# Kernel optimization log

Hardware: AMD Instinct MI355X
Metric: run time of the kernel (lower is better)

The kernel has to match this reference:

```python
import jax, jax.numpy as jnp
import numpy as np

N, I, H = 32, 64, 128
B, T = 16, 256


def setup_inputs() -> dict:
    key = jax.random.key(0)
    k1, k2, k3, k4, k5 = jax.random.split(key, 5)
    stdv = 1.0 / np.sqrt(H)
    x = jax.random.normal(k1, (B, T, N * I), dtype=jnp.float32)
    h0 = jnp.zeros((1, B, N * H), dtype=jnp.float32)
    c0 = jnp.zeros((1, B, N * H), dtype=jnp.float32)
    # Block-diagonal weights stored as batched per-block matrices.
    # weight_ih block i is [4H, I], weight_hh block i is [4H, H].
    weight_ih = jax.random.uniform(k2, (N, 4 * H, I), jnp.float32, -stdv, stdv)
    weight_hh = jax.random.uniform(k3, (N, 4 * H, H), jnp.float32, -stdv, stdv)
    bias_ih = jax.random.uniform(k4, (N, 4 * H), jnp.float32, -stdv, stdv)
    bias_hh = jax.random.uniform(k5, (N, 4 * H), jnp.float32, -stdv, stdv)
    return {"x": x, "h0": h0, "c0": c0, "weight_ih": weight_ih,
            "weight_hh": weight_hh, "bias_ih": bias_ih, "bias_hh": bias_hh}


def _wide_lstm(x, h0, c0, weight_ih, weight_hh, bias_ih, bias_hh):
    b, t, _ = x.shape
    xb = x.reshape(b, t, N, I)
    # Precompute input-to-gate projections for all timesteps: [B,T,N,4H]
    gates_x = jnp.einsum('btni,ngi->btng', xb, weight_ih) + bias_ih
    h_t = h0[0].reshape(b, N, H)
    c_t = c0[0].reshape(b, N, H)

    def step(carry, gx_t):
        h, c = carry
        gates_h = jnp.einsum('bnh,ngh->bng', h, weight_hh) + bias_hh
        gates = gx_t + gates_h  # [B,N,4H]
        i_g = jax.nn.sigmoid(gates[..., 0 * H:1 * H])
        f_g = jax.nn.sigmoid(gates[..., 1 * H:2 * H])
        g_g = jnp.tanh(gates[..., 2 * H:3 * H])
        o_g = jax.nn.sigmoid(gates[..., 3 * H:4 * H])
        c_new = f_g * c + i_g * g_g
        h_new = o_g * jnp.tanh(c_new)
        return (h_new, c_new), h_new

    (h_n, c_n), outs = jax.lax.scan(step, (h_t, c_t),
                                    jnp.swapaxes(gates_x, 0, 1))  # scan over T
    output = jnp.swapaxes(outs, 0, 1).reshape(b, t, N * H)
    return output, h_n.reshape(1, b, N * H), c_n.reshape(1, b, N * H)


def reference(x, h0, c0, weight_ih, weight_hh, bias_ih, bias_hh):
    return _wide_lstm(x, h0, c0, weight_ih, weight_hh, bias_ih, bias_hh)
```

## Files before the change

### kernel.cpp

```cpp
#include <hip/hip_runtime.h>
#include <hip/hip_bf16.h>
#include <cstdint>
#include <cstddef>


#define TSTEPS 256

typedef float  f32x4  __attribute__((ext_vector_type(4)));
typedef float  f32x2  __attribute__((ext_vector_type(2)));
typedef __bf16 bf16x8 __attribute__((ext_vector_type(8)));
typedef short  s16x8  __attribute__((ext_vector_type(8)));

union Frag { s16x8 s; bf16x8 b; };

#define KSIG -1.4426950408889634f
#define KTAN  2.8853900817779268f

__device__ __forceinline__ short f2bf(float f) {
  uint32_t u = __builtin_bit_cast(uint32_t, f);
  u += 0x7fffu + ((u >> 16) & 1u);
  return (short)(u >> 16);
}

__device__ __forceinline__ void sync_lds() {
  asm volatile("s_waitcnt lgkmcnt(0)" ::: "memory");
  __builtin_amdgcn_s_barrier();
  asm volatile("" ::: "memory");
}

__device__ __forceinline__ float sig2(float z) {
  return __builtin_amdgcn_rcpf(1.f + __builtin_amdgcn_exp2f(z));
}

__device__ __forceinline__ f32x4 mf(const Frag a, const Frag bb, f32x4 c) {
  return __builtin_amdgcn_mfma_f32_16x16x32_bf16(a.b, bb.b, c, 0, 0, 0);
}

__global__ __launch_bounds__(512, 2) void wide_lstm(
    const float* __restrict__ x,   const float* __restrict__ h0,
    const float* __restrict__ c0,  const float* __restrict__ wih,
    const float* __restrict__ whh, const float* __restrict__ bih,
    const float* __restrict__ bhh, float* __restrict__ out)
{
  const int n    = blockIdx.x & 31;
  const int bg   = blockIdx.x >> 5;
  const int tid  = threadIdx.x;
  const int w    = tid >> 6;
  const int lane = tid & 63;
  const int col  = lane & 15;
  const int quad = lane >> 4;
  const int b4   = col & 3;
  const int e2   = col >> 2;
  const int hloc = 4 * quad + e2;
  const int hgl  = 16 * w + hloc;
  const int b    = 4 * bg + b4;

  __shared__ alignas(16) short hbuf[2][4 * 144];
  __shared__ alignas(16) short xbuf[2][4 * 96];

  Frag wfr[6][4];
#pragma unroll
  for (int j = 0; j < 4; ++j) {
    const int g = 128 * j + 16 * w + col;
#pragma unroll
    for (int s = 0; s < 6; ++s) {
      const int k0 = 32 * s + quad * 8;
      const float* p = (s < 2) ? (wih + (size_t)(n * 512 + g) * 64  + k0)
                               : (whh + (size_t)(n * 512 + g) * 128 + (k0 - 64));
      const f32x4 lo = *(const f32x4*)p;
      const f32x4 hi = *(const f32x4*)(p + 4);
      Frag f;
      f.s[0]=f2bf(lo[0]); f.s[1]=f2bf(lo[1]); f.s[2]=f2bf(lo[2]); f.s[3]=f2bf(lo[3]);
      f.s[4]=f2bf(hi[0]); f.s[5]=f2bf(hi[1]); f.s[6]=f2bf(hi[2]); f.s[7]=f2bf(hi[3]);
      wfr[s][j] = f;
    }
  }

  f32x4 cb[4];
#pragma unroll
  for (int j = 0; j < 4; ++j) {
    const int base = n * 512 + 128 * j + 16 * w + quad * 4;
    const f32x4 b1 = *(const f32x4*)(bih + base);
    const f32x4 b2 = *(const f32x4*)(bhh + base);
#pragma unroll
    for (int r = 0; r < 4; ++r) cb[j][r] = b1[r] + b2[r];
  }
  const f32x4 kzero = (f32x4){0.f, 0.f, 0.f, 0.f};

  if (tid < 256) {
    const int bi = tid >> 6, j2 = (tid & 63) * 2;
    const f32x2 hv = *(const f32x2*)(h0 + (size_t)(4 * bg + bi) * 4096 + n * 128 + j2);
    *(uint32_t*)&hbuf[0][bi * 144 + j2] =
        (uint32_t)(uint16_t)f2bf(hv[0]) | ((uint32_t)(uint16_t)f2bf(hv[1]) << 16);
  }
  const int bq = tid >> 6;
  const int kq = tid & 63;
  const float* xp = x + (size_t)(4 * bg + bq) * (TSTEPS * 2048) + n * 64 + kq;
  float xr = 0.f;
  if (tid < 256) {
    xbuf[0][bq * 96 + kq] = f2bf(xp[0]);
    xr = xp[2048];
  }
  const float* xnext = xp + 2 * 2048;
  float cg = c0[(size_t)b * 4096 + n * 128 + hgl];
  __syncthreads();

  const int xoff  = b4 * 96  + quad * 8;
  const int hoff  = b4 * 144 + quad * 8;
  const int sxoff = bq * 96 + kq;
  const int hwoff = b4 * 144 + hgl;
  float* outp = out + (size_t)b * (TSTEPS * 4096) + n * 128 + hgl;
  float ho = 0.f;
  const bool m1 = (e2 & 1), m2 = (e2 & 2);

#define LSTM_STEP(CUR, NXT, S)                                               \
  {                                                                          \
    Frag bf[6];                                                              \
    bf[0].s = *(const s16x8*)&xbuf[CUR][xoff];                               \
    bf[1].s = *(const s16x8*)&xbuf[CUR][xoff + 32];                          \
    bf[2].s = *(const s16x8*)&hbuf[CUR][hoff];                               \
    bf[3].s = *(const s16x8*)&hbuf[CUR][hoff + 32];                          \
    bf[4].s = *(const s16x8*)&hbuf[CUR][hoff + 64];                          \
    bf[5].s = *(const s16x8*)&hbuf[CUR][hoff + 96];                          \
    if (tid < 256) {                                                         \
      xbuf[NXT][sxoff] = f2bf(xr);                                           \
      if ((S) + 2 < TSTEPS) { xr = *xnext; xnext += 2048; }                  \
    }                                                                        \
    f32x4 ac1[4], ac2[4];                                                    \
    _Pragma("unroll") for (int j = 0; j < 4; ++j) {                          \
      ac1[j] = mf(wfr[0][j], bf[0], cb[j]);                                  \
      ac2[j] = mf(wfr[3][j], bf[3], kzero);                                  \
    }                                                                        \
    _Pragma("unroll") for (int j = 0; j < 4; ++j) {                          \
      ac1[j] = mf(wfr[1][j], bf[1], ac1[j]);                                 \
      ac2[j] = mf(wfr[4][j], bf[4], ac2[j]);                                 \
    }                                                                        \
    _Pragma("unroll") for (int j = 0; j < 4; ++j) {                          \
      ac1[j] = mf(wfr[2][j], bf[2], ac1[j]);                                 \
      ac2[j] = mf(wfr[5][j], bf[5], ac2[j]);                                 \
    }                                                                        \
    float pre[4];                                                            \
    _Pragma("unroll") for (int j = 0; j < 4; ++j) {                          \
      const float u01 = m1 ? ac1[j][1] : ac1[j][0];                          \
      const float u23 = m1 ? ac1[j][3] : ac1[j][2];                          \
      const float v01 = m1 ? ac2[j][1] : ac2[j][0];                          \
      const float v23 = m1 ? ac2[j][3] : ac2[j][2];                          \
      pre[j] = (m2 ? u23 : u01) + (m2 ? v23 : v01);                          \
    }                                                                        \
    const float si = sig2(KSIG * pre[0]);                                    \
    const float sf = sig2(KSIG * pre[1]);                                    \
    const float sg = sig2(KTAN * pre[2]);                                    \
    const float so = sig2(KSIG * pre[3]);                                    \
    float cn = __builtin_fmaf(sf, cg, si);                                   \
    cn = __builtin_fmaf(-2.f, si * sg, cn);                                  \
    cg = cn;                                                                 \
    ho = so * __builtin_fmaf(-2.f, sig2(KTAN * cn), 1.f);                    \
    hbuf[NXT][hwoff] = f2bf(ho);                                             \
    *outp = ho;                                                              \
    outp += 4096;                                                            \
    sync_lds();                                                              \
  }

  for (int t = 0; t < TSTEPS; t += 2) {
    LSTM_STEP(0, 1, t);
    LSTM_STEP(1, 0, t + 1);
  }
#undef LSTM_STEP

  out[16777216 +         (size_t)b * 4096 + n * 128 + hgl] = ho;
  out[16777216 + 65536 + (size_t)b * 4096 + n * 128 + hgl] = cg;
}

extern "C" void kernel_launch(void* const* d_in, const int* in_sizes, int n_in,
                              void* d_out, int out_size, void* d_ws, size_t ws_size,
                              hipStream_t stream) {
  const float* x   = (const float*)d_in[0];
  const float* h0  = (const float*)d_in[1];
  const float* c0  = (const float*)d_in[2];
  const float* wih = (const float*)d_in[3];
  const float* whh = (const float*)d_in[4];
  const float* bih = (const float*)d_in[5];
  const float* bhh = (const float*)d_in[6];
  float* out = (float*)d_out;
  wide_lstm<<<128, 512, 0, stream>>>(x, h0, c0, wih, whh, bih, bhh, out);
}
```

Baseline: 290.7 us.

## Compute next step's input-projection MFMAs off the recurrent critical path

Moves the x·W_ih MFMAs for timestep t+1 so they run after the current step's gate activations, overlapping with the activation math. The recurrent chain then carries only the four h·W_hh MFMA chains between barriers. The x staging buffer is shifted one step ahead and prologue code computes the first step's input projection directly from global memory. The cost is extra accumulator registers and a sched_barrier that limits compiler reordering.

```diff
diff --git a/kernel.cpp b/kernel.cpp
--- a/kernel.cpp
+++ b/kernel.cpp
@@ -98,11 +98,31 @@
   const float* xp = x + (size_t)(4 * bg + bq) * (TSTEPS * 2048) + n * 64 + kq;
   float xr = 0.f;
   if (tid < 256) {
-    xbuf[0][bq * 96 + kq] = f2bf(xp[0]);
-    xr = xp[2048];
-  }
-  const float* xnext = xp + 2 * 2048;
+    xbuf[1][bq * 96 + kq] = f2bf(xp[2048]);
+    xr = xp[2 * 2048];
+  }
+  const float* xnext = xp + 3 * 2048;
   float cg = c0[(size_t)b * 4096 + n * 128 + hgl];
+
+  f32x4 acpre[4];
+  {
+    const float* q = x + (size_t)b * (TSTEPS * 2048) + n * 64 + 8 * quad;
+    const f32x4 a0 = *(const f32x4*)q;
+    const f32x4 a1 = *(const f32x4*)(q + 4);
+    const f32x4 a2 = *(const f32x4*)(q + 32);
+    const f32x4 a3 = *(const f32x4*)(q + 36);
+    Frag xf0, xf1;
+#pragma unroll
+    for (int r = 0; r < 4; ++r) {
+      xf0.s[r]     = f2bf(a0[r]);
+      xf0.s[4 + r] = f2bf(a1[r]);
+      xf1.s[r]     = f2bf(a2[r]);
+      xf1.s[4 + r] = f2bf(a3[r]);
+    }
+#pragma unroll
+    for (int j = 0; j < 4; ++j)
+      acpre[j] = mf(wfr[1][j], xf1, mf(wfr[0][j], xf0, cb[j]));
+  }
   __syncthreads();
 
   const int xoff  = b4 * 96  + quad * 8;
@@ -115,30 +135,28 @@
 
 #define LSTM_STEP(CUR, NXT, S)                                               \
   {                                                                          \
-    Frag bf[6];                                                              \
-    bf[0].s = *(const s16x8*)&xbuf[CUR][xoff];                               \
-    bf[1].s = *(const s16x8*)&xbuf[CUR][xoff + 32];                          \
-    bf[2].s = *(const s16x8*)&hbuf[CUR][hoff];                               \
-    bf[3].s = *(const s16x8*)&hbuf[CUR][hoff + 32];                          \
-    bf[4].s = *(const s16x8*)&hbuf[CUR][hoff + 64];                          \
-    bf[5].s = *(const s16x8*)&hbuf[CUR][hoff + 96];                          \
+    Frag hf0, hf1, hf2, hf3;                                                 \
+    hf0.s = *(const s16x8*)&hbuf[CUR][hoff];                                 \
+    hf1.s = *(const s16x8*)&hbuf[CUR][hoff + 32];                            \
+    hf2.s = *(const s16x8*)&hbuf[CUR][hoff + 64];                            \
+    hf3.s = *(const s16x8*)&hbuf[CUR][hoff + 96];                            \
     if (tid < 256) {                                                         \
-      xbuf[NXT][sxoff] = f2bf(xr);                                           \
-      if ((S) + 2 < TSTEPS) { xr = *xnext; xnext += 2048; }                  \
+      xbuf[CUR][sxoff] = f2bf(xr);                                           \
+      if ((S) + 3 < TSTEPS) { xr = *xnext; xnext += 2048; }                  \
     }                                                                        \
     f32x4 ac1[4], ac2[4];                                                    \
     _Pragma("unroll") for (int j = 0; j < 4; ++j) {                          \
-      ac1[j] = mf(wfr[0][j], bf[0], cb[j]);                                  \
-      ac2[j] = mf(wfr[3][j], bf[3], kzero);                                  \
+      ac1[j] = mf(wfr[2][j], hf0, acpre[j]);                                 \
+      ac2[j] = mf(wfr[4][j], hf2, kzero);                                    \
     }                                                                        \
     _Pragma("unroll") for (int j = 0; j < 4; ++j) {                          \
-      ac1[j] = mf(wfr[1][j], bf[1], ac1[j]);                                 \
-      ac2[j] = mf(wfr[4][j], bf[4], ac2[j]);                                 \
-    }                                                                        \
-    _Pragma("unroll") for (int j = 0; j < 4; ++j) {                          \
-      ac1[j] = mf(wfr[2][j], bf[2], ac1[j]);                                 \
-      ac2[j] = mf(wfr[5][j], bf[5], ac2[j]);                                 \
-    }                                                                        \
+      ac1[j] = mf(wfr[3][j], hf1, ac1[j]);                                   \
+      ac2[j] = mf(wfr[5][j], hf3, ac2[j]);                                   \
+    }                                                                        \
+    __builtin_amdgcn_sched_barrier(0);  \
+    Frag xg0, xg1;                                                           \
+    xg0.s = *(const s16x8*)&xbuf[NXT][xoff];                                 \
+    xg1.s = *(const s16x8*)&xbuf[NXT][xoff + 32];                            \
     float pre[4];                                                            \
     _Pragma("unroll") for (int j = 0; j < 4; ++j) {                          \
       const float u01 = m1 ? ac1[j][1] : ac1[j][0];                          \
@@ -155,6 +173,10 @@
     cn = __builtin_fmaf(-2.f, si * sg, cn);                                  \
     cg = cn;                                                                 \
     ho = so * __builtin_fmaf(-2.f, sig2(KTAN * cn), 1.f);                    \
+    _Pragma("unroll") for (int j = 0; j < 4; ++j)                            \
+      acpre[j] = mf(wfr[0][j], xg0, cb[j]);                                  \
+    _Pragma("unroll") for (int j = 0; j < 4; ++j)                            \
+      acpre[j] = mf(wfr[1][j], xg1, acpre[j]);                               \
     hbuf[NXT][hwoff] = f2bf(ho);                                             \
     *outp = ho;                                                              \
     outp += 4096;                                                            \
```

After: 292.2 us. About the same (+0.5%).
